# Kernel tuning notes

Hardware: AMD Instinct MI355X
Metric: run time of the kernel (lower is better)

## Reference

```python
import jax, jax.numpy as jnp
import numpy as np

N_NODES = 4096
BATCH = 512
N_EDGES = 131072  # avg degree 32
MAX_STEPS = 120
LEAK = 0.01


def mml(x, leak):
    # Michaelis-Menten-like: leak*x for x<0, x for 0<=x<=0.5, 1 - 0.25/x for x>0.5
    y = jnp.where(x < 0.0, leak * x, x)
    return jnp.where(x > 0.5, 1.0 - 0.25 / jnp.maximum(x, 0.5), y)


def setup_inputs() -> dict:
    key = jax.random.key(0)
    k_tgt, k_src, k_sign, k_val, k_x = jax.random.split(key, 5)
    # edge_list: row0 = target indices, row1 = source indices
    tgt = jax.random.randint(k_tgt, (N_EDGES,), 0, N_NODES)
    src = jax.random.randint(k_src, (N_EDGES,), 0, N_NODES)
    # edge_weights: row0 stimulating, row1 inhibiting (mutually exclusive)
    inhib = jax.random.bernoulli(k_sign, 0.3, (N_EDGES,))
    # initialize_weight_values: 0.1 + 0.1*rand, negated for inhibiting edges
    vals = 0.1 + 0.1 * jax.random.uniform(k_val, (N_EDGES,), dtype=jnp.float32)
    vals = jnp.where(inhib, -vals, vals)
    # dense masked adjacency (non-edges stay exactly 0, as masked_fill_ enforces)
    weights = jnp.zeros((N_NODES, N_NODES), dtype=jnp.float32).at[tgt, src].set(vals)
    # bias: 0.001 everywhere, except 1.0 at targets whose incoming edges are all inhibiting
    any_pos = jax.ops.segment_max(jnp.where(vals > 0, 1, 0), tgt, num_segments=N_NODES)
    has_edge = jax.ops.segment_sum(jnp.ones_like(tgt), tgt, num_segments=N_NODES) > 0
    bias_vec = jnp.where(has_edge & (any_pos == 0), 1.0, 0.001).astype(jnp.float32)
    bias = bias_vec[:, None]  # (N_NODES, 1)
    X_full = jax.random.uniform(k_x, (BATCH, N_NODES), dtype=jnp.float32)
    return {"X_full": X_full, "weights": weights, "bias": bias}


def reference(X_full, weights, bias):
    X_bias = X_full.T + bias  # (n_nodes, batch)

    def step(X, _):
        X = mml(weights @ X + X_bias, LEAK)
        return X, None

    X_ss, _ = jax.lax.scan(step, jnp.zeros_like(X_bias), None, length=MAX_STEPS)
    return X_ss.T  # (batch, n_nodes) steady state
```

## Files before the change

### kernel.cpp

```cpp
#include <hip/hip_runtime.h>
#include <hip/hip_fp16.h>
#include <stdint.h>

#define N_NODES 4096
#define BATCH   512
#define STEPS   120
#define LEAK    0.01f
#define NMASK   4095u
#define MAXG    19
#define ALLOCG  20
#define NN4     N_NODES
#define SCHED_SLOTS 80

#define OFF_DEG    0
#define OFF_CURSOR 16384
#define OFF_HIST   32768
#define OFF_CNT    33792
#define OFF_GMAX   34816
#define OFF_BOUNDS 35072
#define OFF_START  35328
#define OFF_POS    36352
#define OFF_ORIG   52736
#define OFF_E      69632
#define WS_BYTES   (OFF_E + ALLOCG * N_NODES * 16)
#define WS_WORDS   (WS_BYTES / 4)

__global__ void zero_ws(unsigned* __restrict__ p, int n) {
    int i = (int)(blockIdx.x * 1024 + threadIdx.x);
    if (i < n) p[i] = 0u;
}

__global__ void count_deg(const float4* __restrict__ W4, int* __restrict__ deg) {
    int i = (int)(blockIdx.x * 256 + threadIdx.x);
    float4 w = W4[i];
    int nz = (w.x != 0.0f) + (w.y != 0.0f) + (w.z != 0.0f) + (w.w != 0.0f);
    if (nz) atomicAdd(&deg[(i * 4) >> 12], nz);
}

__global__ void hist_deg(const int* __restrict__ deg, int* __restrict__ hist) {
    int t = (int)(blockIdx.x * 256 + threadIdx.x);
    int d = deg[t]; if (d > 255) d = 255;
    atomicAdd(&hist[d], 1);
}

__global__ void scan_start(const int* __restrict__ hist, int* __restrict__ start) {
    __shared__ int sm[256];
    int tid = (int)threadIdx.x;
    int v = hist[tid];
    sm[tid] = v;
    __syncthreads();
    for (int o = 1; o < 256; o <<= 1) {
        int u = (tid >= o) ? sm[tid - o] : 0;
        __syncthreads();
        sm[tid] += u;
        __syncthreads();
    }
    start[tid] = sm[tid] - v;
}

__global__ void rank_assign(const int* __restrict__ deg,
                            const int* __restrict__ start,
                            int* __restrict__ cnt,
                            int* __restrict__ pos_of,
                            int* __restrict__ orig_of,
                            int* __restrict__ gmax) {
    int t = (int)(blockIdx.x * 256 + threadIdx.x);
    int d = deg[t]; int dc = d > 255 ? 255 : d;
    int r = start[dc] + atomicAdd(&cnt[dc], 1);
    int p;
    if      (r < 1024) p = r;
    else if (r < 2048) p = 1024 + (2047 - r);
    else if (r < 3072) p = 2048 + (r - 2048);
    else               p = 3072 + (4095 - r);
    pos_of[t] = p;
    orig_of[p] = t;
    atomicMax(&gmax[p >> 6], d);
}

__global__ void finalize_bounds(const int* __restrict__ gmax,
                                int* __restrict__ bounds) {
    int i = (int)threadIdx.x;
    int g = (gmax[i] + 3) >> 2;
    if (g < 8)    g = 8;
    if (g > MAXG) g = MAXG;
    bounds[i] = g;
}

__global__ void scatter_edges(const float4* __restrict__ W4,
                              const int* __restrict__ pos_of,
                              int* __restrict__ cursor,
                              unsigned* __restrict__ E) {
    int i = (int)(blockIdx.x * 256 + threadIdx.x);
    float4 w = W4[i];
    float v[4] = {w.x, w.y, w.z, w.w};
    int nz = (v[0] != 0.0f) + (v[1] != 0.0f) + (v[2] != 0.0f) + (v[3] != 0.0f);
    if (!nz) return;
    int idx0 = i * 4;
    int t = idx0 >> 12;
    unsigned p = (unsigned)pos_of[t];
    int k = atomicAdd(&cursor[t], nz);
    #pragma unroll
    for (int j = 0; j < 4; ++j) {
        if (v[j] != 0.0f) {
            if (k < MAXG * 4) {
                unsigned sI = (unsigned)(idx0 + j) & NMASK;
                unsigned hw = (unsigned)__half_as_ushort(__float2half(v[j]));
                E[(((unsigned)(k >> 2) * N_NODES + p) << 2) | (unsigned)(k & 3)]
                    = (hw << 16) | ((unsigned)pos_of[sI] << 2);
            }
            ++k;
        }
    }
}

__device__ __forceinline__ int idxB_of(int s) {
    return (s & ~31) | ((s + (s >> 5)) & 31);
}
__device__ __forceinline__ int idxC_of(int s) {
    return (s & ~31) | ((s + 2 * (s >> 5) + 1) & 31);
}

__device__ __forceinline__ void choices_of(unsigned s, unsigned lrot,
                                           int r[3], unsigned a[3]) {
    unsigned iB = (unsigned)idxB_of((int)s);
    unsigned iC = (unsigned)idxC_of((int)s);
    a[0] = s << 2;
    a[1] = 0x4000u | (iB << 2);
    a[2] = 0x8000u | (iC << 2);
    r[0] = (int)(((s  & 31u) - lrot) & 31u);
    r[1] = (int)(((iB & 31u) - lrot) & 31u);
    r[2] = (int)(((iC & 31u) - lrot) & 31u);
}

__global__ void __launch_bounds__(64)
bank_schedule(unsigned* __restrict__ E, const int* __restrict__ bounds) {
    __shared__ unsigned       slotP[64 * SCHED_SLOTS];
    __shared__ unsigned short slotS[64 * SCHED_SLOTS];
    __shared__ unsigned       stageb[64 * SCHED_SLOTS];
    __shared__ int            usedb[64 * 32];
    unsigned*       sp = &slotP[threadIdx.x * SCHED_SLOTS];
    unsigned short* ss = &slotS[threadIdx.x * SCHED_SLOTS];
    unsigned*       st = &stageb[threadIdx.x * SCHED_SLOTS];
    int*            us = &usedb[threadIdx.x * 32];
    int p = (int)(blockIdx.x * 64 + threadIdx.x);
    int B = p >> 10, sl = (p >> 6) & 15;
    int T = bounds[B * 16 + sl] * 4;
    unsigned lrot = (unsigned)(p & 31);

    for (int t = 0; t < T; ++t)
        st[t] = E[(((unsigned)(t >> 2) * NN4 + (unsigned)p) << 2) | (unsigned)(t & 3)];

    for (int t = 0; t < T; ++t) { sp[t] = 0xFFFFFFFFu; ss[t] = 0xFFFF; }
    #pragma unroll
    for (int r = 0; r < 32; ++r) us[r] = 0;

    int novf = 0;
    for (int i = 0; i < T; ++i) {
        unsigned e = st[i];
        if (!(e >> 16)) continue;
        unsigned s = (e >> 2) & NMASK;
        unsigned w = e & 0xFFFF0000u;
        int r[3]; unsigned a[3]; choices_of(s, lrot, r, a);
        int best = -1, smax = 0;
        #pragma unroll
        for (int c = 0; c < 3; ++c) {
            int slack = ((T + 31 - r[c]) >> 5) - us[r[c]];
            if (slack > smax) { smax = slack; best = c; }
        }
        if (best >= 0) {
            int q = r[best];
            sp[q + 32 * us[q]] = w | a[best];
            ss[q + 32 * us[q]] = (unsigned short)s;
            us[q]++;
        } else { st[novf++] = w | (s << 2); }
    }

    int nrem = 0;
    for (int i = 0; i < novf; ++i) {
        unsigned e = st[i];
        unsigned s = (e >> 2) & NMASK;
        unsigned w = e & 0xFFFF0000u;
        int r[3]; unsigned a[3]; choices_of(s, lrot, r, a);
        bool placed = false;
        for (int c = 0; c < 3 && !placed; ++c) {
            int q = r[c], cap = (T + 31 - q) >> 5;
            for (int k = 0; k < cap && !placed; ++k) {
                int t2 = q + 32 * k;
                unsigned s2 = ss[t2];
                if (s2 == 0xFFFF) continue;
                int r2[3]; unsigned a2[3]; choices_of(s2, lrot, r2, a2);
                #pragma unroll
                for (int c2 = 0; c2 < 3; ++c2) {
                    int q2 = r2[c2]; if (q2 == q) continue;
                    int cap2 = (T + 31 - q2) >> 5;
                    if (us[q2] < cap2) {
                        unsigned w2 = sp[t2] & 0xFFFF0000u;
                        sp[q2 + 32 * us[q2]] = w2 | a2[c2];
                        ss[q2 + 32 * us[q2]] = (unsigned short)s2;
                        us[q2]++;
                        sp[t2] = w | a[c]; ss[t2] = (unsigned short)s;
                        placed = true; break;
                    }
                }
            }
        }
        if (!placed) { st[nrem++] = e; }
    }

    int oi = 0;
    for (int t = 0; t < T; ++t) {
        if (sp[t] != 0xFFFFFFFFu) continue;
        if (oi < nrem) { sp[t] = st[oi++]; }
        else sp[t] = ((((unsigned)p & ~31u) | (((unsigned)p + (unsigned)t) & 31u)) << 2);
    }
    for (int t = 0; t < T; ++t)
        E[(((unsigned)(t >> 2) * NN4 + (unsigned)p) << 2) | (unsigned)(t & 3)] = sp[t];
}

__device__ __forceinline__ float mml_f(float x) {
    float y = (x < 0.0f) ? (LEAK * x) : x;
    if (x > 0.5f) y = 1.0f - 0.25f / x;
    return y;
}
__device__ __forceinline__ __half2 mml_pack2(float ax, float ay) {
    return __floats2half2_rn(mml_f(ax), mml_f(ay));
}

#define EMIX(U, XW, AX, AY)                                                  \
    asm("v_fma_mix_f32 %0, %1, %2, %0 op_sel:[1,0,0] op_sel_hi:[1,1,0]"      \
        : "+v"(AX) : "v"(U), "v"(XW));                                       \
    asm("v_fma_mix_f32 %0, %1, %2, %0 op_sel:[1,1,0] op_sel_hi:[1,1,0]"      \
        : "+v"(AY) : "v"(U), "v"(XW));

#define EDGE4(C, S, AX, AY) {                                                \
    unsigned _x0 = *(const unsigned*)((const char*)(S) + ((C).x & 0xFFFCu)); \
    unsigned _x1 = *(const unsigned*)((const char*)(S) + ((C).y & 0xFFFCu)); \
    unsigned _x2 = *(const unsigned*)((const char*)(S) + ((C).z & 0xFFFCu)); \
    unsigned _x3 = *(const unsigned*)((const char*)(S) + ((C).w & 0xFFFCu)); \
    EMIX((C).x, _x0, AX, AY) EMIX((C).y, _x1, AX, AY)                        \
    EMIX((C).z, _x2, AX, AY) EMIX((C).w, _x3, AX, AY) }

#define STEP(S, D) {                                                         \
    float a0x = xb0.x, a0y = xb0.y, a1x = xb1.x, a1y = xb1.y;                \
    float a2x = xb2.x, a2y = xb2.y, a3x = xb3.x, a3y = xb3.y;                \
    uint4 c0 = B0[0], c1 = B1[0], c2 = B2[0], c3 = B3[0];                    \
    int g = 0;                                                               \
    for (; g < Gm; ++g) {                                                    \
        uint4 n0 = B0[(size_t)(g + 1) * NN4], n1 = B1[(size_t)(g + 1) * NN4];\
        uint4 n2 = B2[(size_t)(g + 1) * NN4], n3 = B3[(size_t)(g + 1) * NN4];\
        EDGE4(c0, S, a0x, a0y) EDGE4(c1, S, a1x, a1y)                        \
        EDGE4(c2, S, a2x, a2y) EDGE4(c3, S, a3x, a3y)                        \
        c0 = n0; c1 = n1; c2 = n2; c3 = n3;                                  \
    }                                                                        \
    for (int h = g; h < G0; ++h) {                                           \
        uint4 n = B0[(size_t)(h + 1) * NN4]; EDGE4(c0, S, a0x, a0y) c0 = n; }\
    for (int h = g; h < G1; ++h) {                                           \
        uint4 n = B1[(size_t)(h + 1) * NN4]; EDGE4(c1, S, a1x, a1y) c1 = n; }\
    for (int h = g; h < G2; ++h) {                                           \
        uint4 n = B2[(size_t)(h + 1) * NN4]; EDGE4(c2, S, a2x, a2y) c2 = n; }\
    for (int h = g; h < G3; ++h) {                                           \
        uint4 n = B3[(size_t)(h + 1) * NN4]; EDGE4(c3, S, a3x, a3y) c3 = n; }\
    __half2 v0 = mml_pack2(a0x, a0y), v1 = mml_pack2(a1x, a1y);              \
    __half2 v2 = mml_pack2(a2x, a2y), v3 = mml_pack2(a3x, a3y);              \
    (D)[tid]        = v0; (D)[4096 + ib0] = v0; (D)[8192 + ic0] = v0;        \
    (D)[1024 + tid] = v1; (D)[4096 + ib1] = v1; (D)[8192 + ic1] = v1;        \
    (D)[2048 + tid] = v2; (D)[4096 + ib2] = v2; (D)[8192 + ic2] = v2;        \
    (D)[3072 + tid] = v3; (D)[4096 + ib3] = v3; (D)[8192 + ic3] = v3;        \
    __syncthreads(); }

__global__ void __launch_bounds__(1024, 4)
iterate_kernel(const float* __restrict__ X_full,
               const float* __restrict__ bias,
               const unsigned* __restrict__ E,
               const int* __restrict__ bounds,
               const int* __restrict__ orig_of,
               float* __restrict__ out) {
    __shared__ __half2 sbuf[2 * 12288];
    __half2* buf0 = sbuf;
    __half2* buf1 = sbuf + 12288;

    const int tid  = (int)threadIdx.x;
    const int colb = (int)blockIdx.x * 2;
    const int s    = tid >> 6;
    const uint4* Eb = (const uint4*)E;

    const int G0 = bounds[s],      G1 = bounds[16 + s];
    const int G2 = bounds[32 + s], G3 = bounds[48 + s];
    const int Gm = min(min(G0, G1), min(G2, G3));

    const uint4* B0 = Eb + tid;
    const uint4* B1 = Eb + 1024 + tid;
    const uint4* B2 = Eb + 2048 + tid;
    const uint4* B3 = Eb + 3072 + tid;

    const int ib0 = idxB_of(tid),        ib1 = idxB_of(1024 + tid);
    const int ib2 = idxB_of(2048 + tid), ib3 = idxB_of(3072 + tid);
    const int ic0 = idxC_of(tid),        ic1 = idxC_of(1024 + tid);
    const int ic2 = idxC_of(2048 + tid), ic3 = idxC_of(3072 + tid);

    const int t0 = orig_of[tid],        t1 = orig_of[1024 + tid];
    const int t2 = orig_of[2048 + tid], t3 = orig_of[3072 + tid];

    const float* x0r = X_full + (size_t)colb * N_NODES;
    const float* x1r = x0r + N_NODES;
    float b0 = bias[t0], b1 = bias[t1], b2 = bias[t2], b3 = bias[t3];
    float2 xb0 = make_float2(x0r[t0] + b0, x1r[t0] + b0);
    float2 xb1 = make_float2(x0r[t1] + b1, x1r[t1] + b1);
    float2 xb2 = make_float2(x0r[t2] + b2, x1r[t2] + b2);
    float2 xb3 = make_float2(x0r[t3] + b3, x1r[t3] + b3);

    {
        __half2 v0 = mml_pack2(xb0.x, xb0.y), v1 = mml_pack2(xb1.x, xb1.y);
        __half2 v2 = mml_pack2(xb2.x, xb2.y), v3 = mml_pack2(xb3.x, xb3.y);
        buf0[tid]        = v0; buf0[4096 + ib0] = v0; buf0[8192 + ic0] = v0;
        buf0[1024 + tid] = v1; buf0[4096 + ib1] = v1; buf0[8192 + ic1] = v1;
        buf0[2048 + tid] = v2; buf0[4096 + ib2] = v2; buf0[8192 + ic2] = v2;
        buf0[3072 + tid] = v3; buf0[4096 + ib3] = v3; buf0[8192 + ic3] = v3;
    }
    __syncthreads();

    #pragma unroll 1
    for (int p = 0; p < 59; ++p) {
        STEP(buf0, buf1)
        STEP(buf1, buf0)
    }
    STEP(buf0, buf1)

    __half2 f0 = buf1[tid],        f1 = buf1[1024 + tid];
    __half2 f2 = buf1[2048 + tid], f3 = buf1[3072 + tid];
    float* o0 = out + (size_t)colb * N_NODES;
    float* o1 = o0 + N_NODES;
    o0[t0] = __low2float(f0);  o0[t1] = __low2float(f1);
    o0[t2] = __low2float(f2);  o0[t3] = __low2float(f3);
    o1[t0] = __high2float(f0); o1[t1] = __high2float(f1);
    o1[t2] = __high2float(f2); o1[t3] = __high2float(f3);
}

extern "C" void kernel_launch(void* const* d_in, const int* in_sizes, int n_in,
                              void* d_out, int out_size, void* d_ws, size_t ws_size,
                              hipStream_t stream) {
    const float* X_full = nullptr;
    const float* W      = nullptr;
    const float* bias   = nullptr;
    for (int i = 0; i < n_in; ++i) {
        if      (in_sizes[i] == N_NODES * N_NODES) W      = (const float*)d_in[i];
        else if (in_sizes[i] == BATCH * N_NODES)   X_full = (const float*)d_in[i];
        else if (in_sizes[i] == N_NODES)           bias   = (const float*)d_in[i];
    }

    char* ws = (char*)d_ws;
    int*      deg    = (int*)(ws + OFF_DEG);
    int*      cursor = (int*)(ws + OFF_CURSOR);
    int*      hist   = (int*)(ws + OFF_HIST);
    int*      cnt    = (int*)(ws + OFF_CNT);
    int*      gmax   = (int*)(ws + OFF_GMAX);
    int*      bounds = (int*)(ws + OFF_BOUNDS);
    int*      start  = (int*)(ws + OFF_START);
    int*      pos_of = (int*)(ws + OFF_POS);
    int*      orig   = (int*)(ws + OFF_ORIG);
    unsigned* E      = (unsigned*)(ws + OFF_E);

    zero_ws        <<<(WS_WORDS + 1023) / 1024, 1024, 0, stream>>>((unsigned*)ws, WS_WORDS);
    count_deg      <<<N_NODES * N_NODES / 4 / 256, 256, 0, stream>>>((const float4*)W, deg);
    hist_deg       <<<N_NODES / 256, 256, 0, stream>>>(deg, hist);
    scan_start     <<<1, 256, 0, stream>>>(hist, start);
    rank_assign    <<<N_NODES / 256, 256, 0, stream>>>(deg, start, cnt, pos_of, orig, gmax);
    finalize_bounds<<<1, 64, 0, stream>>>(gmax, bounds);
    scatter_edges  <<<N_NODES * N_NODES / 4 / 256, 256, 0, stream>>>((const float4*)W, pos_of, cursor, E);
    bank_schedule  <<<N_NODES / 64, 64, 0, stream>>>(E, bounds);
    iterate_kernel <<<BATCH / 2, 1024, 0, stream>>>(X_full, bias, E, bounds, orig,
                                                    (float*)d_out);
}
```

Baseline: 989.2 us.

## Wave-aggregate atomics, shrink zeroing, lower group floor, merge tail loops

Several independent changes. count_deg and scatter_edges now reduce or scan within each wavefront so one atomic is issued per wave instead of per thread. zero_ws now clears only the metadata region and no longer the edge buffer, with bank_schedule reading only the true per-node degree from a new pdeg array so stale entries are never read. The minimum group count drops from 8 to 4. The iterate loop is unrolled by 2, and the four per-row tail loops are merged into one predicated loop. These cut setup memory traffic and atomic contention, but the per-degree loop bounds depend on the bank schedule padding unused slots correctly.

```diff
diff --git a/kernel.cpp b/kernel.cpp
--- a/kernel.cpp
+++ b/kernel.cpp
@@ -21,9 +21,10 @@
 #define OFF_START  35328
 #define OFF_POS    36352
 #define OFF_ORIG   52736
-#define OFF_E      69632
+#define OFF_PDEG   69632
+#define OFF_E      86016
 #define WS_BYTES   (OFF_E + ALLOCG * N_NODES * 16)
-#define WS_WORDS   (WS_BYTES / 4)
+#define ZERO_WORDS (OFF_E / 4)
 
 __global__ void zero_ws(unsigned* __restrict__ p, int n) {
     int i = (int)(blockIdx.x * 1024 + threadIdx.x);
@@ -34,7 +35,10 @@
     int i = (int)(blockIdx.x * 256 + threadIdx.x);
     float4 w = W4[i];
     int nz = (w.x != 0.0f) + (w.y != 0.0f) + (w.z != 0.0f) + (w.w != 0.0f);
-    if (nz) atomicAdd(&deg[(i * 4) >> 12], nz);
+    #pragma unroll
+    for (int o = 32; o > 0; o >>= 1) nz += __shfl_down(nz, o);
+    if ((threadIdx.x & 63) == 0 && nz)
+        atomicAdd(&deg[(i * 4) >> 12], nz);
 }
 
 __global__ void hist_deg(const int* __restrict__ deg, int* __restrict__ hist) {
@@ -63,7 +67,8 @@
                             int* __restrict__ cnt,
                             int* __restrict__ pos_of,
                             int* __restrict__ orig_of,
-                            int* __restrict__ gmax) {
+                            int* __restrict__ gmax,
+                            int* __restrict__ pdeg) {
     int t = (int)(blockIdx.x * 256 + threadIdx.x);
     int d = deg[t]; int dc = d > 255 ? 255 : d;
     int r = start[dc] + atomicAdd(&cnt[dc], 1);
@@ -74,6 +79,7 @@
     else               p = 3072 + (4095 - r);
     pos_of[t] = p;
     orig_of[p] = t;
+    pdeg[p] = d;
     atomicMax(&gmax[p >> 6], d);
 }
 
@@ -81,7 +87,7 @@
                                 int* __restrict__ bounds) {
     int i = (int)threadIdx.x;
     int g = (gmax[i] + 3) >> 2;
-    if (g < 8)    g = 8;
+    if (g < 4)    g = 4;
     if (g > MAXG) g = MAXG;
     bounds[i] = g;
 }
@@ -94,18 +100,28 @@
     float4 w = W4[i];
     float v[4] = {w.x, w.y, w.z, w.w};
     int nz = (v[0] != 0.0f) + (v[1] != 0.0f) + (v[2] != 0.0f) + (v[3] != 0.0f);
-    if (!nz) return;
     int idx0 = i * 4;
     int t = idx0 >> 12;
+    int lane = (int)(threadIdx.x & 63);
+    int inc = nz;
+    #pragma unroll
+    for (int o = 1; o < 64; o <<= 1) {
+        int u = __shfl_up(inc, o);
+        if (lane >= o) inc += u;
+    }
+    int base = 0;
+    if (lane == 63 && inc > 0) base = atomicAdd(&cursor[t], inc);
+    base = __shfl(base, 63);
+    if (!nz) return;
+    int k = base + inc - nz;
     unsigned p = (unsigned)pos_of[t];
-    int k = atomicAdd(&cursor[t], nz);
     #pragma unroll
     for (int j = 0; j < 4; ++j) {
         if (v[j] != 0.0f) {
             if (k < MAXG * 4) {
                 unsigned sI = (unsigned)(idx0 + j) & NMASK;
                 unsigned hw = (unsigned)__half_as_ushort(__float2half(v[j]));
-                E[(((unsigned)(k >> 2) * N_NODES + p) << 2) | (unsigned)(k & 3)]
+                E[(((unsigned)(k >> 2) * NN4 + p) << 2) | (unsigned)(k & 3)]
                     = (hw << 16) | ((unsigned)pos_of[sI] << 2);
             }
             ++k;
@@ -133,7 +149,8 @@
 }
 
 __global__ void __launch_bounds__(64)
-bank_schedule(unsigned* __restrict__ E, const int* __restrict__ bounds) {
+bank_schedule(unsigned* __restrict__ E, const int* __restrict__ bounds,
+              const int* __restrict__ pdeg) {
     __shared__ unsigned       slotP[64 * SCHED_SLOTS];
     __shared__ unsigned short slotS[64 * SCHED_SLOTS];
     __shared__ unsigned       stageb[64 * SCHED_SLOTS];
@@ -145,9 +162,10 @@
     int p = (int)(blockIdx.x * 64 + threadIdx.x);
     int B = p >> 10, sl = (p >> 6) & 15;
     int T = bounds[B * 16 + sl] * 4;
+    int pd = pdeg[p]; if (pd > T) pd = T;
     unsigned lrot = (unsigned)(p & 31);
 
-    for (int t = 0; t < T; ++t)
+    for (int t = 0; t < pd; ++t)
         st[t] = E[(((unsigned)(t >> 2) * NN4 + (unsigned)p) << 2) | (unsigned)(t & 3)];
 
     for (int t = 0; t < T; ++t) { sp[t] = 0xFFFFFFFFu; ss[t] = 0xFFFF; }
@@ -155,9 +173,8 @@
     for (int r = 0; r < 32; ++r) us[r] = 0;
 
     int novf = 0;
-    for (int i = 0; i < T; ++i) {
+    for (int i = 0; i < pd; ++i) {
         unsigned e = st[i];
-        if (!(e >> 16)) continue;
         unsigned s = (e >> 2) & NMASK;
         unsigned w = e & 0xFFFF0000u;
         int r[3]; unsigned a[3]; choices_of(s, lrot, r, a);
@@ -245,6 +262,7 @@
     float a2x = xb2.x, a2y = xb2.y, a3x = xb3.x, a3y = xb3.y;                \
     uint4 c0 = B0[0], c1 = B1[0], c2 = B2[0], c3 = B3[0];                    \
     int g = 0;                                                               \
+    _Pragma("unroll 2")                                                      \
     for (; g < Gm; ++g) {                                                    \
         uint4 n0 = B0[(size_t)(g + 1) * NN4], n1 = B1[(size_t)(g + 1) * NN4];\
         uint4 n2 = B2[(size_t)(g + 1) * NN4], n3 = B3[(size_t)(g + 1) * NN4];\
@@ -252,14 +270,17 @@
         EDGE4(c2, S, a2x, a2y) EDGE4(c3, S, a3x, a3y)                        \
         c0 = n0; c1 = n1; c2 = n2; c3 = n3;                                  \
     }                                                                        \
-    for (int h = g; h < G0; ++h) {                                           \
-        uint4 n = B0[(size_t)(h + 1) * NN4]; EDGE4(c0, S, a0x, a0y) c0 = n; }\
-    for (int h = g; h < G1; ++h) {                                           \
-        uint4 n = B1[(size_t)(h + 1) * NN4]; EDGE4(c1, S, a1x, a1y) c1 = n; }\
-    for (int h = g; h < G2; ++h) {                                           \
-        uint4 n = B2[(size_t)(h + 1) * NN4]; EDGE4(c2, S, a2x, a2y) c2 = n; }\
-    for (int h = g; h < G3; ++h) {                                           \
-        uint4 n = B3[(size_t)(h + 1) * NN4]; EDGE4(c3, S, a3x, a3y) c3 = n; }\
+    for (int h = g; h < Gx; ++h) {                                           \
+        uint4 n0, n1, n2, n3;                                                \
+        if (h < G0) n0 = B0[(size_t)(h + 1) * NN4];                          \
+        if (h < G1) n1 = B1[(size_t)(h + 1) * NN4];                          \
+        if (h < G2) n2 = B2[(size_t)(h + 1) * NN4];                          \
+        if (h < G3) n3 = B3[(size_t)(h + 1) * NN4];                          \
+        if (h < G0) { EDGE4(c0, S, a0x, a0y) c0 = n0; }                      \
+        if (h < G1) { EDGE4(c1, S, a1x, a1y) c1 = n1; }                      \
+        if (h < G2) { EDGE4(c2, S, a2x, a2y) c2 = n2; }                      \
+        if (h < G3) { EDGE4(c3, S, a3x, a3y) c3 = n3; }                      \
+    }                                                                        \
     __half2 v0 = mml_pack2(a0x, a0y), v1 = mml_pack2(a1x, a1y);              \
     __half2 v2 = mml_pack2(a2x, a2y), v3 = mml_pack2(a3x, a3y);              \
     (D)[tid]        = v0; (D)[4096 + ib0] = v0; (D)[8192 + ic0] = v0;        \
@@ -287,6 +308,7 @@
     const int G0 = bounds[s],      G1 = bounds[16 + s];
     const int G2 = bounds[32 + s], G3 = bounds[48 + s];
     const int Gm = min(min(G0, G1), min(G2, G3));
+    const int Gx = max(max(G0, G1), max(G2, G3));
 
     const uint4* B0 = Eb + tid;
     const uint4* B1 = Eb + 1024 + tid;
@@ -352,22 +374,23 @@
     int*      deg    = (int*)(ws + OFF_DEG);
     int*      cursor = (int*)(ws + OFF_CURSOR);
     int*      hist   = (int*)(ws + OFF_HIST);
+    int*      start  = (int*)(ws + OFF_START);
     int*      cnt    = (int*)(ws + OFF_CNT);
     int*      gmax   = (int*)(ws + OFF_GMAX);
     int*      bounds = (int*)(ws + OFF_BOUNDS);
-    int*      start  = (int*)(ws + OFF_START);
     int*      pos_of = (int*)(ws + OFF_POS);
     int*      orig   = (int*)(ws + OFF_ORIG);
+    int*      pdeg   = (int*)(ws + OFF_PDEG);
     unsigned* E      = (unsigned*)(ws + OFF_E);
 
-    zero_ws        <<<(WS_WORDS + 1023) / 1024, 1024, 0, stream>>>((unsigned*)ws, WS_WORDS);
+    zero_ws        <<<(ZERO_WORDS + 1023) / 1024, 1024, 0, stream>>>((unsigned*)ws, ZERO_WORDS);
     count_deg      <<<N_NODES * N_NODES / 4 / 256, 256, 0, stream>>>((const float4*)W, deg);
     hist_deg       <<<N_NODES / 256, 256, 0, stream>>>(deg, hist);
     scan_start     <<<1, 256, 0, stream>>>(hist, start);
-    rank_assign    <<<N_NODES / 256, 256, 0, stream>>>(deg, start, cnt, pos_of, orig, gmax);
+    rank_assign    <<<N_NODES / 256, 256, 0, stream>>>(deg, start, cnt, pos_of, orig, gmax, pdeg);
     finalize_bounds<<<1, 64, 0, stream>>>(gmax, bounds);
     scatter_edges  <<<N_NODES * N_NODES / 4 / 256, 256, 0, stream>>>((const float4*)W, pos_of, cursor, E);
-    bank_schedule  <<<N_NODES / 64, 64, 0, stream>>>(E, bounds);
+    bank_schedule  <<<N_NODES / 64, 64, 0, stream>>>(E, bounds, pdeg);
     iterate_kernel <<<BATCH / 2, 1024, 0, stream>>>(X_full, bias, E, bounds, orig,
                                                     (float*)d_out);
 }
```

Result: no change. 992.5 us (+0.3%).
